# Kernel tuning notes

Measured on AMD Instinct MI355X. Metric: run time of the kernel, lower is better.

## Reference

```python
import jax, jax.numpy as jnp
import numpy as np

T = 16384       # tokens (flattened leading dims)
D_IN = 1024     # in_features
D_OUT = 1024    # out_features
E = 8           # n_models (experts)


def setup_inputs() -> dict:
    key = jax.random.key(0)
    kx, ki, kw, kb = jax.random.split(key, 4)
    x = jax.random.normal(kx, (T, D_IN), dtype=jnp.float32)
    idxs = jax.random.randint(ki, (T,), 0, E, dtype=jnp.int32)
    # Per-expert Linear params (nn.Linear default-ish init scale)
    scale = 1.0 / np.sqrt(D_IN)
    W = jax.random.uniform(kw, (E, D_IN, D_OUT), dtype=jnp.float32, minval=-scale, maxval=scale)
    b = jax.random.uniform(kb, (E, D_OUT), dtype=jnp.float32, minval=-scale, maxval=scale)
    return {"x": x, "idxs": idxs, "W": W, "b": b}


def reference(x, idxs, W, b):
    # Original: for each expert i, y[idxs==i] = Linear_i(x[idxs==i]); return relu(y).
    # Equivalent math: each token t gets expert idxs[t]'s linear.
    # Compute all experts densely (E is small), then gather the assigned row.
    ys = jnp.einsum('ti,eio->eto', x, W) + b[:, None, :]   # [E, T, D_OUT]
    y = ys[idxs, jnp.arange(x.shape[0])]                    # [T, D_OUT] pick assigned expert
    return jax.nn.relu(y)
```

## Files before the change

### kernel.cpp

```cpp
#include <hip/hip_runtime.h>
#include <hip/hip_bf16.h>
#include <stdint.h>


#define T_TOK 16384
#define DIN   1024
#define DOUT  1024
#define NE    8
#define BM    128
#define BN    64
#define BK    64
#define TPX   17
#define MAX_TILES 136
#define MP_MAX (T_TOK + NE * BM)

typedef __attribute__((ext_vector_type(8))) short short8;
typedef __attribute__((ext_vector_type(4))) short short4v;
typedef __attribute__((ext_vector_type(4))) float floatx4;
typedef __attribute__((ext_vector_type(4))) int int4v;

__device__ __forceinline__ short f2b(float f) {
  return __builtin_bit_cast(short, __float2bfloat16(f));
}
__device__ __forceinline__ float b2f(unsigned short u) {
  unsigned v = ((unsigned)u) << 16;
  return __builtin_bit_cast(float, v);
}
__device__ __forceinline__ void glds16(const void* g, void* l) {
  __builtin_amdgcn_global_load_lds(
      (__attribute__((address_space(1))) void*)g,
      (__attribute__((address_space(3))) void*)l, 16, 0, 0);
}

#define FLAG_OFF    0
#define NTILES_OFF  64
#define COUNTS_OFF  128
#define PADOFF_OFF  512
#define BB_OFF      1024
#define TABLE_OFF   4096
#define TPAD_OFF    8192
#define WT_OFF      81920
#define APERM_OFF   16859136
#define WS_NEED     (16859136UL + (size_t)MP_MAX * DIN * 2)

__global__ void k_prep(const unsigned short* __restrict__ x, const int* __restrict__ idxs,
                       int* __restrict__ flag, int* __restrict__ countsG,
                       int* __restrict__ padoffG, int* __restrict__ ntiles,
                       int4v* __restrict__ table, int* __restrict__ blockBase,
                       int* __restrict__ tpad) {
  __shared__ int wtot[16][NE];
  __shared__ int waveBase[16][NE];
  __shared__ int totS[NE], padS[NE + 1];
  int tid = threadIdx.x;
  int lane = tid & 63, w = tid >> 6;

  if (tid < 64) {
    int f = 0;
    #pragma unroll
    for (int i = 0; i < 4; ++i) {
      int ex = (x[tid * 4 + i] >> 7) & 0xFF;
      if (ex >= 0xC0) f = 1;
    }
    unsigned long long any = __ballot(f);
    if (tid == 0) *flag = any ? 1 : 0;
  }

  int c[NE];
  #pragma unroll
  for (int e = 0; e < NE; ++e) c[e] = 0;
  const int4v* iv = (const int4v*)idxs;
  #pragma unroll
  for (int it = 0; it < 4; ++it) {
    int4v v = iv[tid * 4 + it];
    ++c[v.x]; ++c[v.y]; ++c[v.z]; ++c[v.w];
  }
  int incl[NE];
  #pragma unroll
  for (int e = 0; e < NE; ++e) {
    incl[e] = c[e];
    #pragma unroll
    for (int d = 1; d < 64; d <<= 1) {
      int o = __shfl_up(incl[e], d);
      if (lane >= d) incl[e] += o;
    }
  }
  if (lane == 63) {
    #pragma unroll
    for (int e = 0; e < NE; ++e) wtot[w][e] = incl[e];
  }
  __syncthreads();
  if (tid < NE) {
    int s = 0;
    for (int ww = 0; ww < 16; ++ww) s += wtot[ww][tid];
    totS[tid] = s;
    countsG[tid] = s;
  }
  __syncthreads();
  if (tid == 0) {
    int p = 0, tc = 0;
    for (int e = 0; e < NE; ++e) {
      padS[e] = p;
      padoffG[e] = p;
      int cn = totS[e];
      int nmt = (cn + BM - 1) >> 7;
      for (int m = 0; m < nmt; ++m) table[tc++] = (int4v){e, p + m * BM, 0, 0};
      p += nmt * BM;
    }
    padS[NE] = p;
    padoffG[NE] = p;
    *ntiles = tc;
  }
  __syncthreads();
  if (tid < 128) {
    int ww = tid >> 3, e = tid & 7;
    int s = padS[e];
    for (int wp = 0; wp < ww; ++wp) s += wtot[wp][e];
    waveBase[ww][e] = s;
  }
  __syncthreads();
  if ((tid & 15) == 0) {
    int B = tid >> 4;
    #pragma unroll
    for (int e = 0; e < NE; ++e)
      blockBase[B * NE + e] = waveBase[w][e] + (incl[e] - c[e]);
  }
  #pragma unroll
  for (int e = 0; e < NE; ++e) {
    int start = padS[e] + totS[e];
    int len = padS[e + 1] - start;
    if (tid < len) tpad[start + tid] = -1;
  }
}

__global__ void k_scatter(const int* __restrict__ idxs, const int* __restrict__ blockBase,
                          int* __restrict__ tpad) {
  __shared__ int wc[4][NE], wexcl[4][NE];
  int b = blockIdx.x, tid = threadIdx.x;
  int lane = tid & 63, w = tid >> 6;
  int t = b * 256 + tid;
  int e = idxs[t];
  unsigned long long mymask = 0;
  #pragma unroll
  for (int e0 = 0; e0 < NE; ++e0) {
    unsigned long long m = __ballot(e == e0);
    if (lane == 0) wc[w][e0] = __popcll(m);
    if (e0 == e) mymask = m;
  }
  int rw = __popcll(mymask & ((1ull << lane) - 1ull));
  __syncthreads();
  if (tid < 32) {
    int ww = tid >> 3, e0 = tid & 7;
    int s = 0;
    for (int wp = 0; wp < ww; ++wp) s += wc[wp][e0];
    wexcl[ww][e0] = s;
  }
  __syncthreads();
  tpad[blockBase[b * NE + e] + wexcl[w][e] + rw] = t;
}

#define TRANS_BLOCKS (NE * 16 * 16)
#define GATHER_BLOCKS (MP_MAX / 4)
__global__ void k_stage(const void* __restrict__ Wsrc, short* __restrict__ Wt,
                        const void* __restrict__ xv, short* __restrict__ Aperm,
                        const int* __restrict__ padoffG, const int* __restrict__ tpad,
                        const int* __restrict__ flagp) {
  int tid = threadIdx.x;
  int fp32 = *flagp;
  if (blockIdx.x < TRANS_BLOCKS) {
    __shared__ unsigned short tile[64][66];
    int b = blockIdx.x;
    int e = b >> 8;
    int kt = (b >> 4) & 15;
    int nt = b & 15;
    size_t ibase = (size_t)e * DIN * DOUT + (size_t)(kt * 64) * DOUT + nt * 64;
    #pragma unroll
    for (int it = 0; it < 2; ++it) {
      int c = it * 256 + tid;
      int k = c >> 3, n8 = (c & 7) * 8;
      short8 v;
      if (fp32) {
        const float* p = (const float*)Wsrc + ibase + (size_t)k * DOUT + n8;
        floatx4 a = *(const floatx4*)p;
        floatx4 b4 = *(const floatx4*)(p + 4);
        v[0]=f2b(a[0]); v[1]=f2b(a[1]); v[2]=f2b(a[2]); v[3]=f2b(a[3]);
        v[4]=f2b(b4[0]); v[5]=f2b(b4[1]); v[6]=f2b(b4[2]); v[7]=f2b(b4[3]);
      } else {
        v = *(const short8*)((const short*)Wsrc + ibase + (size_t)k * DOUT + n8);
      }
      #pragma unroll
      for (int jj = 0; jj < 8; ++jj) tile[k][n8 + jj] = (unsigned short)v[jj];
    }
    __syncthreads();
    size_t obase = (size_t)e * DOUT * DIN + (size_t)(nt * 64) * DIN + kt * 64;
    #pragma unroll
    for (int it = 0; it < 2; ++it) {
      int c = it * 256 + tid;
      int n = c >> 3, k8 = (c & 7) * 8;
      short8 o;
      #pragma unroll
      for (int jj = 0; jj < 8; ++jj) o[jj] = (short)tile[k8 + jj][n];
      *(short8*)(Wt + obase + (size_t)n * DIN + k8) = o;
    }
    return;
  }
  int mp = padoffG[NE];
  int rb = (blockIdx.x - TRANS_BLOCKS) * 4 + (tid >> 6);
  int lane = tid & 63;
  if (rb >= mp) return;
  int tok = tpad[rb];
  short8 v0 = {0, 0, 0, 0, 0, 0, 0, 0}, v1 = v0;
  if (tok >= 0) {
    if (fp32) {
      const float* xf = (const float*)xv + (size_t)tok * DIN + lane * 16;
      floatx4 a = *(const floatx4*)xf;
      floatx4 b = *(const floatx4*)(xf + 4);
      floatx4 c = *(const floatx4*)(xf + 8);
      floatx4 d = *(const floatx4*)(xf + 12);
      v0[0]=f2b(a[0]); v0[1]=f2b(a[1]); v0[2]=f2b(a[2]); v0[3]=f2b(a[3]);
      v0[4]=f2b(b[0]); v0[5]=f2b(b[1]); v0[6]=f2b(b[2]); v0[7]=f2b(b[3]);
      v1[0]=f2b(c[0]); v1[1]=f2b(c[1]); v1[2]=f2b(c[2]); v1[3]=f2b(c[3]);
      v1[4]=f2b(d[0]); v1[5]=f2b(d[1]); v1[6]=f2b(d[2]); v1[7]=f2b(d[3]);
    } else {
      const short* xs = (const short*)xv + (size_t)tok * DIN + lane * 16;
      v0 = *(const short8*)xs;
      v1 = *(const short8*)(xs + 8);
    }
  }
  short* dst = Aperm + (size_t)rb * DIN + lane * 16;
  *(short8*)dst = v0;
  *(short8*)(dst + 8) = v1;
}

__launch_bounds__(256, 6)
__global__ void k_gemm(const short* __restrict__ Aperm, const void* __restrict__ bv,
                       const short* __restrict__ Wt, const int* __restrict__ tpad,
                       const int* __restrict__ ntilesp, const int4v* __restrict__ table,
                       const int* __restrict__ flagp, void* __restrict__ outv) {
  int bid = blockIdx.x;
  int xcd = bid & 7;
  int s = bid >> 3;
  int nt = s & 15;
  int ti = s >> 4;
  int t = xcd * TPX + ti;
  if (t >= *ntilesp) return;
  int4v te = table[t];
  int e = te.x, arow0 = te.y;
  int fp32 = *flagp;

  int tid = threadIdx.x;
  int lane = tid & 63;
  int wave = tid >> 6;

  __shared__ short lA[BM * BK];
  __shared__ short lB[BN * BK];
  __shared__ int tokS[BM];

  const short* WtE = Wt + (size_t)e * DOUT * DIN + (size_t)(nt * BN) * DIN;
  const short* aBase = Aperm + (size_t)arow0 * DIN;

  const short* aG[4];
  char* aL[4];
  #pragma unroll
  for (int s4 = 0; s4 < 4; ++s4) {
    int fl = tid + s4 * 256;
    int r = fl >> 3, p = fl & 7;
    int kc = p ^ (r & 7);
    aG[s4] = aBase + (size_t)r * DIN + kc * 8;
    aL[s4] = (char*)lA + (s4 * 256 + wave * 64) * 16;
  }
  const short* bG[2];
  char* bL[2];
  #pragma unroll
  for (int s4 = 0; s4 < 2; ++s4) {
    int fl = tid + s4 * 256;
    int r = fl >> 3, p = fl & 7;
    int kc = p ^ (r & 7);
    bG[s4] = WtE + (size_t)r * DIN + kc * 8;
    bL[s4] = (char*)lB + (s4 * 256 + wave * 64) * 16;
  }

  int wm = wave & 1, wn = wave >> 1;
  int lrow = lane & 15, q = lane >> 4;
  int aOff[4][2], bOff[2][2];
  #pragma unroll
  for (int i = 0; i < 4; ++i) {
    int m = wm * 64 + i * 16 + lrow;
    #pragma unroll
    for (int h = 0; h < 2; ++h)
      aOff[i][h] = m * BK + (((h * 4 + q) ^ (m & 7)) * 8);
  }
  #pragma unroll
  for (int j = 0; j < 2; ++j) {
    int n = wn * 32 + j * 16 + lrow;
    #pragma unroll
    for (int h = 0; h < 2; ++h)
      bOff[j][h] = n * BK + (((h * 4 + q) ^ (n & 7)) * 8);
  }

  floatx4 acc[4][2];
  #pragma unroll
  for (int i = 0; i < 4; ++i)
    #pragma unroll
    for (int j = 0; j < 2; ++j)
      acc[i][j] = (floatx4){0.f, 0.f, 0.f, 0.f};

  for (int k0 = 0; k0 < DIN; k0 += BK) {
    __syncthreads();
    #pragma unroll
    for (int s4 = 0; s4 < 2; ++s4) glds16(bG[s4] + k0, bL[s4]);
    #pragma unroll
    for (int s4 = 0; s4 < 4; ++s4) glds16(aG[s4] + k0, aL[s4]);
    __syncthreads();
    #pragma unroll
    for (int h = 0; h < 2; ++h) {
      short8 af[4], bf[2];
      #pragma unroll
      for (int i = 0; i < 4; ++i) af[i] = *(const short8*)(lA + aOff[i][h]);
      #pragma unroll
      for (int j = 0; j < 2; ++j) bf[j] = *(const short8*)(lB + bOff[j][h]);
      #pragma unroll
      for (int i = 0; i < 4; ++i)
        #pragma unroll
        for (int j = 0; j < 2; ++j)
          acc[i][j] = __builtin_amdgcn_mfma_f32_16x16x32_bf16(bf[j], af[i], acc[i][j], 0, 0, 0);
    }
  }

  if (tid < BM) tokS[tid] = tpad[arow0 + tid];
  __syncthreads();

  float bias[2][4];
  #pragma unroll
  for (int j = 0; j < 2; ++j) {
    int n = nt * BN + wn * 32 + j * 16 + q * 4;
    if (fp32) {
      floatx4 b4 = *(const floatx4*)((const float*)bv + e * DOUT + n);
      #pragma unroll
      for (int r = 0; r < 4; ++r) bias[j][r] = b4[r];
    } else {
      short4v b4 = *(const short4v*)((const short*)bv + e * DOUT + n);
      #pragma unroll
      for (int r = 0; r < 4; ++r) bias[j][r] = b2f((unsigned short)b4[r]);
    }
  }
  #pragma unroll
  for (int i = 0; i < 4; ++i) {
    int tok = tokS[wm * 64 + i * 16 + lrow];
    if (tok < 0) continue;
    size_t rowb = (size_t)tok * DOUT + nt * BN + wn * 32 + q * 4;
    #pragma unroll
    for (int j = 0; j < 2; ++j) {
      if (fp32) {
        floatx4 o;
        #pragma unroll
        for (int r = 0; r < 4; ++r) {
          float v = acc[i][j][r] + bias[j][r];
          o[r] = v > 0.f ? v : 0.f;
        }
        *(floatx4*)((float*)outv + rowb + j * 16) = o;
      } else {
        short4v o;
        #pragma unroll
        for (int r = 0; r < 4; ++r) {
          float v = acc[i][j][r] + bias[j][r];
          o[r] = f2b(v > 0.f ? v : 0.f);
        }
        *(short4v*)((short*)outv + rowb + j * 16) = o;
      }
    }
  }
}

__global__ void k_fallback(const void* __restrict__ xv, const int* __restrict__ idxs,
                           const void* __restrict__ Wv, const void* __restrict__ bv,
                           void* __restrict__ outv) {
  __shared__ float xrow[DIN];
  __shared__ int sflag;
  int t = blockIdx.x;
  int e = idxs[t];
  if (threadIdx.x == 0) {
    const unsigned short* u = (const unsigned short*)xv;
    int f = 0;
    for (int i = 0; i < 256; ++i) { int ex = (u[i] >> 7) & 0xFF; if (ex >= 0xC0) f = 1; }
    sflag = f;
  }
  __syncthreads();
  int fp32 = sflag;
  for (int i = threadIdx.x; i < DIN; i += 256)
    xrow[i] = fp32 ? ((const float*)xv)[(size_t)t * DIN + i]
                   : b2f(((const unsigned short*)xv)[(size_t)t * DIN + i]);
  __syncthreads();
  float a[4] = {0.f, 0.f, 0.f, 0.f};
  for (int k = 0; k < DIN; ++k) {
    float xk = xrow[k];
    size_t wb = (size_t)e * DIN * DOUT + (size_t)k * DOUT + threadIdx.x;
    #pragma unroll
    for (int j = 0; j < 4; ++j) {
      float w = fp32 ? ((const float*)Wv)[wb + j * 256]
                     : b2f(((const unsigned short*)Wv)[wb + j * 256]);
      a[j] += xk * w;
    }
  }
  #pragma unroll
  for (int j = 0; j < 4; ++j) {
    int n = threadIdx.x + j * 256;
    float bias = fp32 ? ((const float*)bv)[e * DOUT + n]
                      : b2f(((const unsigned short*)bv)[e * DOUT + n]);
    float v = a[j] + bias;
    v = v > 0.f ? v : 0.f;
    size_t o = (size_t)t * DOUT + n;
    if (fp32) ((float*)outv)[o] = v;
    else      ((short*)outv)[o] = f2b(v);
  }
}

extern "C" void kernel_launch(void* const* d_in, const int* in_sizes, int n_in,
                              void* d_out, int out_size, void* d_ws, size_t ws_size,
                              hipStream_t stream) {
  const void* x    = d_in[0];
  const int*  idxs = (const int*)d_in[1];
  const void* W    = d_in[2];
  const void* bias = d_in[3];

  if (ws_size < WS_NEED) {
    k_fallback<<<T_TOK, 256, 0, stream>>>(x, idxs, W, bias, d_out);
    return;
  }
  char* ws = (char*)d_ws;
  int* flag    = (int*)(ws + FLAG_OFF);
  int* ntiles  = (int*)(ws + NTILES_OFF);
  int* counts  = (int*)(ws + COUNTS_OFF);
  int* padoff  = (int*)(ws + PADOFF_OFF);
  int* bbase   = (int*)(ws + BB_OFF);
  int4v* table = (int4v*)(ws + TABLE_OFF);
  int* tpad    = (int*)(ws + TPAD_OFF);
  short* Wt    = (short*)(ws + WT_OFF);
  short* Aperm = (short*)(ws + APERM_OFF);

  k_prep<<<1, 1024, 0, stream>>>((const unsigned short*)x, idxs, flag, counts,
                                 padoff, ntiles, table, bbase, tpad);
  k_scatter<<<T_TOK / 256, 256, 0, stream>>>(idxs, bbase, tpad);
  k_stage<<<TRANS_BLOCKS + GATHER_BLOCKS, 256, 0, stream>>>(
      W, Wt, x, Aperm, padoff, tpad, flag);
  k_gemm<<<8 * 16 * TPX, 256, 0, stream>>>(Aperm, bias, Wt, tpad, ntiles, table, flag, d_out);
}
```

Baseline: 213.7 us.

## Fuse prep/scatter/transpose into one kernel and gather x directly in GEMM

Measured after the change: 222.0 us. 3.9% more time.

```diff
diff --git a/kernel.cpp b/kernel.cpp
--- a/kernel.cpp
+++ b/kernel.cpp
@@ -8,7 +8,7 @@
 #define DOUT  1024
 #define NE    8
 #define BM    128
-#define BN    64
+#define BN    128
 #define BK    64
 #define TPX   17
 #define MAX_TILES 136
@@ -34,45 +34,79 @@
 
 #define FLAG_OFF    0
 #define NTILES_OFF  64
-#define COUNTS_OFF  128
-#define PADOFF_OFF  512
-#define BB_OFF      1024
-#define TABLE_OFF   4096
+#define TABLE_OFF   1024
 #define TPAD_OFF    8192
 #define WT_OFF      81920
-#define APERM_OFF   16859136
-#define WS_NEED     (16859136UL + (size_t)MP_MAX * DIN * 2)
-
-__global__ void k_prep(const unsigned short* __restrict__ x, const int* __restrict__ idxs,
-                       int* __restrict__ flag, int* __restrict__ countsG,
-                       int* __restrict__ padoffG, int* __restrict__ ntiles,
-                       int4v* __restrict__ table, int* __restrict__ blockBase,
-                       int* __restrict__ tpad) {
-  __shared__ int wtot[16][NE];
-  __shared__ int waveBase[16][NE];
+#define WS_NEED     (81920UL + (size_t)NE * DIN * DOUT * 2)
+
+__global__ __launch_bounds__(1024) void k_front(
+    const unsigned short* __restrict__ xu, const int* __restrict__ idxs,
+    const void* __restrict__ Wsrc, short* __restrict__ Wt,
+    int* __restrict__ flag, int* __restrict__ ntiles,
+    int4v* __restrict__ table, int* __restrict__ tpad) {
+  __shared__ int fS;
+  __shared__ unsigned short tile[128][130];
+  __shared__ int wtot[16][NE], waveBase[16][NE];
   __shared__ int totS[NE], padS[NE + 1];
+
   int tid = threadIdx.x;
+  if (tid == 0) fS = 0;
+  __syncthreads();
+  if (tid < 256) {
+    int ex = (xu[tid] >> 7) & 0xFF;
+    if (ex >= 0xC0) atomicOr(&fS, 1);
+  }
+  __syncthreads();
+  int fp32 = fS;
+
+  if (blockIdx.x != 0) {
+    int b = blockIdx.x - 1;
+    int e = b >> 6, kt = (b >> 3) & 7, nt8 = b & 7;
+    size_t ibase = (size_t)e * DIN * DOUT + (size_t)(kt * 128) * DOUT + nt8 * 128;
+    int k = tid >> 3, n16 = (tid & 7) * 16;
+    if (fp32) {
+      const float* p = (const float*)Wsrc + ibase + (size_t)k * DOUT + n16;
+      #pragma unroll
+      for (int g = 0; g < 4; ++g) {
+        floatx4 a = *(const floatx4*)(p + g * 4);
+        #pragma unroll
+        for (int j = 0; j < 4; ++j) tile[k][n16 + g * 4 + j] = (unsigned short)f2b(a[j]);
+      }
+    } else {
+      const short* p = (const short*)Wsrc + ibase + (size_t)k * DOUT + n16;
+      #pragma unroll
+      for (int g = 0; g < 2; ++g) {
+        short8 v = *(const short8*)(p + g * 8);
+        #pragma unroll
+        for (int j = 0; j < 8; ++j) tile[k][n16 + g * 8 + j] = (unsigned short)v[j];
+      }
+    }
+    __syncthreads();
+    int n = tid >> 3, k16 = (tid & 7) * 16;
+    short8 o0, o1;
+    #pragma unroll
+    for (int j = 0; j < 8; ++j) {
+      o0[j] = (short)tile[k16 + j][n];
+      o1[j] = (short)tile[k16 + 8 + j][n];
+    }
+    size_t obase = (size_t)e * DOUT * DIN + (size_t)(nt8 * 128 + n) * DIN + kt * 128 + k16;
+    *(short8*)(Wt + obase) = o0;
+    *(short8*)(Wt + obase + 8) = o1;
+    return;
+  }
+
   int lane = tid & 63, w = tid >> 6;
-
-  if (tid < 64) {
-    int f = 0;
-    #pragma unroll
-    for (int i = 0; i < 4; ++i) {
-      int ex = (x[tid * 4 + i] >> 7) & 0xFF;
-      if (ex >= 0xC0) f = 1;
-    }
-    unsigned long long any = __ballot(f);
-    if (tid == 0) *flag = any ? 1 : 0;
-  }
+  if (tid == 0) *flag = fp32;
 
   int c[NE];
   #pragma unroll
   for (int e = 0; e < NE; ++e) c[e] = 0;
   const int4v* iv = (const int4v*)idxs;
+  int4v vv[4];
   #pragma unroll
   for (int it = 0; it < 4; ++it) {
-    int4v v = iv[tid * 4 + it];
-    ++c[v.x]; ++c[v.y]; ++c[v.z]; ++c[v.w];
+    vv[it] = iv[tid * 4 + it];
+    ++c[vv[it].x]; ++c[vv[it].y]; ++c[vv[it].z]; ++c[vv[it].w];
   }
   int incl[NE];
   #pragma unroll
@@ -93,21 +127,18 @@
     int s = 0;
     for (int ww = 0; ww < 16; ++ww) s += wtot[ww][tid];
     totS[tid] = s;
-    countsG[tid] = s;
   }
   __syncthreads();
   if (tid == 0) {
     int p = 0, tc = 0;
     for (int e = 0; e < NE; ++e) {
       padS[e] = p;
-      padoffG[e] = p;
       int cn = totS[e];
       int nmt = (cn + BM - 1) >> 7;
       for (int m = 0; m < nmt; ++m) table[tc++] = (int4v){e, p + m * BM, 0, 0};
       p += nmt * BM;
     }
     padS[NE] = p;
-    padoffG[NE] = p;
     *ntiles = tc;
   }
   __syncthreads();
@@ -118,11 +149,19 @@
     waveBase[ww][e] = s;
   }
   __syncthreads();
-  if ((tid & 15) == 0) {
-    int B = tid >> 4;
-    #pragma unroll
-    for (int e = 0; e < NE; ++e)
-      blockBase[B * NE + e] = waveBase[w][e] + (incl[e] - c[e]);
+  int base[NE];
+  #pragma unroll
+  for (int e = 0; e < NE; ++e) base[e] = waveBase[w][e] + incl[e] - c[e];
+  #pragma unroll
+  for (int it = 0; it < 4; ++it) {
+    #pragma unroll
+    for (int cm = 0; cm < 4; ++cm) {
+      int te = vv[it][cm];
+      int tk = tid * 16 + it * 4 + cm;
+      #pragma unroll
+      for (int e0 = 0; e0 < NE; ++e0)
+        if (te == e0) tpad[base[e0]++] = tk;
+    }
   }
   #pragma unroll
   for (int e = 0; e < NE; ++e) {
@@ -132,115 +171,16 @@
   }
 }
 
-__global__ void k_scatter(const int* __restrict__ idxs, const int* __restrict__ blockBase,
-                          int* __restrict__ tpad) {
-  __shared__ int wc[4][NE], wexcl[4][NE];
-  int b = blockIdx.x, tid = threadIdx.x;
-  int lane = tid & 63, w = tid >> 6;
-  int t = b * 256 + tid;
-  int e = idxs[t];
-  unsigned long long mymask = 0;
-  #pragma unroll
-  for (int e0 = 0; e0 < NE; ++e0) {
-    unsigned long long m = __ballot(e == e0);
-    if (lane == 0) wc[w][e0] = __popcll(m);
-    if (e0 == e) mymask = m;
-  }
-  int rw = __popcll(mymask & ((1ull << lane) - 1ull));
-  __syncthreads();
-  if (tid < 32) {
-    int ww = tid >> 3, e0 = tid & 7;
-    int s = 0;
-    for (int wp = 0; wp < ww; ++wp) s += wc[wp][e0];
-    wexcl[ww][e0] = s;
-  }
-  __syncthreads();
-  tpad[blockBase[b * NE + e] + wexcl[w][e] + rw] = t;
-}
-
-#define TRANS_BLOCKS (NE * 16 * 16)
-#define GATHER_BLOCKS (MP_MAX / 4)
-__global__ void k_stage(const void* __restrict__ Wsrc, short* __restrict__ Wt,
-                        const void* __restrict__ xv, short* __restrict__ Aperm,
-                        const int* __restrict__ padoffG, const int* __restrict__ tpad,
-                        const int* __restrict__ flagp) {
-  int tid = threadIdx.x;
-  int fp32 = *flagp;
-  if (blockIdx.x < TRANS_BLOCKS) {
-    __shared__ unsigned short tile[64][66];
-    int b = blockIdx.x;
-    int e = b >> 8;
-    int kt = (b >> 4) & 15;
-    int nt = b & 15;
-    size_t ibase = (size_t)e * DIN * DOUT + (size_t)(kt * 64) * DOUT + nt * 64;
-    #pragma unroll
-    for (int it = 0; it < 2; ++it) {
-      int c = it * 256 + tid;
-      int k = c >> 3, n8 = (c & 7) * 8;
-      short8 v;
-      if (fp32) {
-        const float* p = (const float*)Wsrc + ibase + (size_t)k * DOUT + n8;
-        floatx4 a = *(const floatx4*)p;
-        floatx4 b4 = *(const floatx4*)(p + 4);
-        v[0]=f2b(a[0]); v[1]=f2b(a[1]); v[2]=f2b(a[2]); v[3]=f2b(a[3]);
-        v[4]=f2b(b4[0]); v[5]=f2b(b4[1]); v[6]=f2b(b4[2]); v[7]=f2b(b4[3]);
-      } else {
-        v = *(const short8*)((const short*)Wsrc + ibase + (size_t)k * DOUT + n8);
-      }
-      #pragma unroll
-      for (int jj = 0; jj < 8; ++jj) tile[k][n8 + jj] = (unsigned short)v[jj];
-    }
-    __syncthreads();
-    size_t obase = (size_t)e * DOUT * DIN + (size_t)(nt * 64) * DIN + kt * 64;
-    #pragma unroll
-    for (int it = 0; it < 2; ++it) {
-      int c = it * 256 + tid;
-      int n = c >> 3, k8 = (c & 7) * 8;
-      short8 o;
-      #pragma unroll
-      for (int jj = 0; jj < 8; ++jj) o[jj] = (short)tile[k8 + jj][n];
-      *(short8*)(Wt + obase + (size_t)n * DIN + k8) = o;
-    }
-    return;
-  }
-  int mp = padoffG[NE];
-  int rb = (blockIdx.x - TRANS_BLOCKS) * 4 + (tid >> 6);
-  int lane = tid & 63;
-  if (rb >= mp) return;
-  int tok = tpad[rb];
-  short8 v0 = {0, 0, 0, 0, 0, 0, 0, 0}, v1 = v0;
-  if (tok >= 0) {
-    if (fp32) {
-      const float* xf = (const float*)xv + (size_t)tok * DIN + lane * 16;
-      floatx4 a = *(const floatx4*)xf;
-      floatx4 b = *(const floatx4*)(xf + 4);
-      floatx4 c = *(const floatx4*)(xf + 8);
-      floatx4 d = *(const floatx4*)(xf + 12);
-      v0[0]=f2b(a[0]); v0[1]=f2b(a[1]); v0[2]=f2b(a[2]); v0[3]=f2b(a[3]);
-      v0[4]=f2b(b[0]); v0[5]=f2b(b[1]); v0[6]=f2b(b[2]); v0[7]=f2b(b[3]);
-      v1[0]=f2b(c[0]); v1[1]=f2b(c[1]); v1[2]=f2b(c[2]); v1[3]=f2b(c[3]);
-      v1[4]=f2b(d[0]); v1[5]=f2b(d[1]); v1[6]=f2b(d[2]); v1[7]=f2b(d[3]);
-    } else {
-      const short* xs = (const short*)xv + (size_t)tok * DIN + lane * 16;
-      v0 = *(const short8*)xs;
-      v1 = *(const short8*)(xs + 8);
-    }
-  }
-  short* dst = Aperm + (size_t)rb * DIN + lane * 16;
-  *(short8*)dst = v0;
-  *(short8*)(dst + 8) = v1;
-}
-
-__launch_bounds__(256, 6)
-__global__ void k_gemm(const short* __restrict__ Aperm, const void* __restrict__ bv,
+__launch_bounds__(256, 3)
+__global__ void k_gemm(const void* __restrict__ xv, const void* __restrict__ bv,
                        const short* __restrict__ Wt, const int* __restrict__ tpad,
                        const int* __restrict__ ntilesp, const int4v* __restrict__ table,
                        const int* __restrict__ flagp, void* __restrict__ outv) {
   int bid = blockIdx.x;
   int xcd = bid & 7;
   int s = bid >> 3;
-  int nt = s & 15;
-  int ti = s >> 4;
+  int nt = s & 7;
+  int ti = s >> 3;
   int t = xcd * TPX + ti;
   if (t >= *ntilesp) return;
   int4v te = table[t];
@@ -251,27 +191,19 @@
   int lane = tid & 63;
   int wave = tid >> 6;
 
-  __shared__ short lA[BM * BK];
+  __shared__ char lA[BM * BK * 4];
   __shared__ short lB[BN * BK];
   __shared__ int tokS[BM];
 
+  if (tid < BM) tokS[tid] = tpad[arow0 + tid];
+  __syncthreads();
+
   const short* WtE = Wt + (size_t)e * DOUT * DIN + (size_t)(nt * BN) * DIN;
-  const short* aBase = Aperm + (size_t)arow0 * DIN;
-
-  const short* aG[4];
-  char* aL[4];
+
+  const short* bG[4];
+  char* bL[4];
   #pragma unroll
   for (int s4 = 0; s4 < 4; ++s4) {
-    int fl = tid + s4 * 256;
-    int r = fl >> 3, p = fl & 7;
-    int kc = p ^ (r & 7);
-    aG[s4] = aBase + (size_t)r * DIN + kc * 8;
-    aL[s4] = (char*)lA + (s4 * 256 + wave * 64) * 16;
-  }
-  const short* bG[2];
-  char* bL[2];
-  #pragma unroll
-  for (int s4 = 0; s4 < 2; ++s4) {
     int fl = tid + s4 * 256;
     int r = fl >> 3, p = fl & 7;
     int kc = p ^ (r & 7);
@@ -281,88 +213,139 @@
 
   int wm = wave & 1, wn = wave >> 1;
   int lrow = lane & 15, q = lane >> 4;
-  int aOff[4][2], bOff[2][2];
-  #pragma unroll
-  for (int i = 0; i < 4; ++i) {
-    int m = wm * 64 + i * 16 + lrow;
-    #pragma unroll
-    for (int h = 0; h < 2; ++h)
-      aOff[i][h] = m * BK + (((h * 4 + q) ^ (m & 7)) * 8);
-  }
-  #pragma unroll
-  for (int j = 0; j < 2; ++j) {
-    int n = wn * 32 + j * 16 + lrow;
+  int bOff[4][2];
+  #pragma unroll
+  for (int j = 0; j < 4; ++j) {
+    int n = wn * 64 + j * 16 + lrow;
     #pragma unroll
     for (int h = 0; h < 2; ++h)
       bOff[j][h] = n * BK + (((h * 4 + q) ^ (n & 7)) * 8);
   }
 
-  floatx4 acc[4][2];
+  floatx4 acc[4][4];
   #pragma unroll
   for (int i = 0; i < 4; ++i)
     #pragma unroll
-    for (int j = 0; j < 2; ++j)
+    for (int j = 0; j < 4; ++j)
       acc[i][j] = (floatx4){0.f, 0.f, 0.f, 0.f};
 
-  for (int k0 = 0; k0 < DIN; k0 += BK) {
-    __syncthreads();
-    #pragma unroll
-    for (int s4 = 0; s4 < 2; ++s4) glds16(bG[s4] + k0, bL[s4]);
-    #pragma unroll
-    for (int s4 = 0; s4 < 4; ++s4) glds16(aG[s4] + k0, aL[s4]);
-    __syncthreads();
-    #pragma unroll
-    for (int h = 0; h < 2; ++h) {
-      short8 af[4], bf[2];
-      #pragma unroll
-      for (int i = 0; i < 4; ++i) af[i] = *(const short8*)(lA + aOff[i][h]);
-      #pragma unroll
-      for (int j = 0; j < 2; ++j) bf[j] = *(const short8*)(lB + bOff[j][h]);
-      #pragma unroll
-      for (int i = 0; i < 4; ++i)
-        #pragma unroll
-        for (int j = 0; j < 2; ++j)
-          acc[i][j] = __builtin_amdgcn_mfma_f32_16x16x32_bf16(bf[j], af[i], acc[i][j], 0, 0, 0);
-    }
-  }
-
-  if (tid < BM) tokS[tid] = tpad[arow0 + tid];
-  __syncthreads();
-
-  float bias[2][4];
-  #pragma unroll
-  for (int j = 0; j < 2; ++j) {
-    int n = nt * BN + wn * 32 + j * 16 + q * 4;
-    if (fp32) {
-      floatx4 b4 = *(const floatx4*)((const float*)bv + e * DOUT + n);
-      #pragma unroll
-      for (int r = 0; r < 4; ++r) bias[j][r] = b4[r];
-    } else {
-      short4v b4 = *(const short4v*)((const short*)bv + e * DOUT + n);
-      #pragma unroll
-      for (int r = 0; r < 4; ++r) bias[j][r] = b2f((unsigned short)b4[r]);
-    }
-  }
+  if (fp32) {
+    const char* aG[8];
+    char* aL[8];
+    #pragma unroll
+    for (int s4 = 0; s4 < 8; ++s4) {
+      int fl = tid + s4 * 256;
+      int r = fl >> 4, p = fl & 15;
+      int lc = p ^ (r & 15);
+      int tok = tokS[r];
+      if (tok < 0) tok = 0;
+      aG[s4] = (const char*)xv + (size_t)tok * (DIN * 4) + lc * 16;
+      aL[s4] = lA + (s4 * 256 + wave * 64) * 16;
+    }
+    int aOff[4][2];
+    #pragma unroll
+    for (int i = 0; i < 4; ++i) {
+      int m = wm * 64 + i * 16 + lrow;
+      #pragma unroll
+      for (int h = 0; h < 2; ++h)
+        aOff[i][h] = m * 256 + ((((h * 4 + q) * 2) ^ (m & 15)) * 16);
+    }
+    for (int k0 = 0; k0 < DIN; k0 += BK) {
+      __syncthreads();
+      #pragma unroll
+      for (int s4 = 0; s4 < 4; ++s4) glds16(bG[s4] + k0, bL[s4]);
+      #pragma unroll
+      for (int s4 = 0; s4 < 8; ++s4) glds16(aG[s4] + k0 * 4, aL[s4]);
+      __syncthreads();
+      #pragma unroll
+      for (int h = 0; h < 2; ++h) {
+        short8 af[4], bf[4];
+        #pragma unroll
+        for (int i = 0; i < 4; ++i) {
+          int a0 = aOff[i][h];
+          floatx4 f0 = *(const floatx4*)(lA + a0);
+          floatx4 f1 = *(const floatx4*)(lA + (a0 ^ 16));
+          short8 v;
+          v[0] = f2b(f0[0]); v[1] = f2b(f0[1]); v[2] = f2b(f0[2]); v[3] = f2b(f0[3]);
+          v[4] = f2b(f1[0]); v[5] = f2b(f1[1]); v[6] = f2b(f1[2]); v[7] = f2b(f1[3]);
+          af[i] = v;
+        }
+        #pragma unroll
+        for (int j = 0; j < 4; ++j) bf[j] = *(const short8*)(lB + bOff[j][h]);
+        #pragma unroll
+        for (int i = 0; i < 4; ++i)
+          #pragma unroll
+          for (int j = 0; j < 4; ++j)
+            acc[i][j] = __builtin_amdgcn_mfma_f32_16x16x32_bf16(bf[j], af[i], acc[i][j], 0, 0, 0);
+      }
+    }
+  } else {
+    const char* aG[4];
+    char* aL[4];
+    #pragma unroll
+    for (int s4 = 0; s4 < 4; ++s4) {
+      int fl = tid + s4 * 256;
+      int r = fl >> 3, p = fl & 7;
+      int kc = p ^ (r & 7);
+      int tok = tokS[r];
+      if (tok < 0) tok = 0;
+      aG[s4] = (const char*)xv + (size_t)tok * (DIN * 2) + kc * 16;
+      aL[s4] = lA + (s4 * 256 + wave * 64) * 16;
+    }
+    int aOff[4][2];
+    #pragma unroll
+    for (int i = 0; i < 4; ++i) {
+      int m = wm * 64 + i * 16 + lrow;
+      #pragma unroll
+      for (int h = 0; h < 2; ++h)
+        aOff[i][h] = m * BK + (((h * 4 + q) ^ (m & 7)) * 8);
+    }
+    for (int k0 = 0; k0 < DIN; k0 += BK) {
+      __syncthreads();
+      #pragma unroll
+      for (int s4 = 0; s4 < 4; ++s4) glds16(bG[s4] + k0, bL[s4]);
+      #pragma unroll
+      for (int s4 = 0; s4 < 4; ++s4) glds16(aG[s4] + k0 * 2, aL[s4]);
+      __syncthreads();
+      #pragma unroll
+      for (int h = 0; h < 2; ++h) {
+        short8 af[4], bf[4];
+        #pragma unroll
+        for (int i = 0; i < 4; ++i) af[i] = *(const short8*)((const short*)lA + aOff[i][h]);
+        #pragma unroll
+        for (int j = 0; j < 4; ++j) bf[j] = *(const short8*)(lB + bOff[j][h]);
+        #pragma unroll
+        for (int i = 0; i < 4; ++i)
+          #pragma unroll
+          for (int j = 0; j < 4; ++j)
+            acc[i][j] = __builtin_amdgcn_mfma_f32_16x16x32_bf16(bf[j], af[i], acc[i][j], 0, 0, 0);
+      }
+    }
+  }
+
   #pragma unroll
   for (int i = 0; i < 4; ++i) {
     int tok = tokS[wm * 64 + i * 16 + lrow];
     if (tok < 0) continue;
-    size_t rowb = (size_t)tok * DOUT + nt * BN + wn * 32 + q * 4;
-    #pragma unroll
-    for (int j = 0; j < 2; ++j) {
+    size_t rowb = (size_t)tok * DOUT + nt * BN + wn * 64 + q * 4;
+    #pragma unroll
+    for (int j = 0; j < 4; ++j) {
+      int n = nt * BN + wn * 64 + j * 16 + q * 4;
       if (fp32) {
+        floatx4 b4 = *(const floatx4*)((const float*)bv + e * DOUT + n);
         floatx4 o;
         #pragma unroll
         for (int r = 0; r < 4; ++r) {
-          float v = acc[i][j][r] + bias[j][r];
+          float v = acc[i][j][r] + b4[r];
           o[r] = v > 0.f ? v : 0.f;
         }
         *(floatx4*)((float*)outv + rowb + j * 16) = o;
       } else {
+        short4v b4 = *(const short4v*)((const short*)bv + e * DOUT + n);
         short4v o;
         #pragma unroll
         for (int r = 0; r < 4; ++r) {
-          float v = acc[i][j][r] + bias[j][r];
+          float v = acc[i][j][r] + b2f((unsigned short)b4[r]);
           o[r] = f2b(v > 0.f ? v : 0.f);
         }
         *(short4v*)((short*)outv + rowb + j * 16) = o;
@@ -429,18 +412,11 @@
   char* ws = (char*)d_ws;
   int* flag    = (int*)(ws + FLAG_OFF);
   int* ntiles  = (int*)(ws + NTILES_OFF);
-  int* counts  = (int*)(ws + COUNTS_OFF);
-  int* padoff  = (int*)(ws + PADOFF_OFF);
-  int* bbase   = (int*)(ws + BB_OFF);
   int4v* table = (int4v*)(ws + TABLE_OFF);
   int* tpad    = (int*)(ws + TPAD_OFF);
   short* Wt    = (short*)(ws + WT_OFF);
-  short* Aperm = (short*)(ws + APERM_OFF);
-
-  k_prep<<<1, 1024, 0, stream>>>((const unsigned short*)x, idxs, flag, counts,
-                                 padoff, ntiles, table, bbase, tpad);
-  k_scatter<<<T_TOK / 256, 256, 0, stream>>>(idxs, bbase, tpad);
-  k_stage<<<TRANS_BLOCKS + GATHER_BLOCKS, 256, 0, stream>>>(
-      W, Wt, x, Aperm, padoff, tpad, flag);
-  k_gemm<<<8 * 16 * TPX, 256, 0, stream>>>(Aperm, bias, Wt, tpad, ntiles, table, flag, d_out);
-}
+
+  k_front<<<1 + NE * 64, 1024, 0, stream>>>((const unsigned short*)x, idxs, W, Wt,
+                                            flag, ntiles, table, tpad);
+  k_gemm<<<8 * 8 * TPX, 256, 0, stream>>>(x, bias, Wt, tpad, ntiles, table, flag, d_out);
+}
```
